# Kernel tuning notes

Hardware: AMD Instinct MI355X
Metric: run time of the kernel (lower is better)

The kernel has to match this reference:

```python
import jax, jax.numpy as jnp
import numpy as np

B, G, D, H = 8, 32, 768, 12
N = G * G
HD = D // H  # 64


def _make_rope(grid_size, head_dim):
    half = head_dim // 2
    inv_freq = 1.0 / (10000.0 ** (jnp.arange(0, half, 2, dtype=jnp.float32) / half))  # [half//2]
    pos = jnp.arange(grid_size, dtype=jnp.float32)[:, None] * inv_freq[None, :]       # [G, half//2]
    emb1 = jnp.concatenate([jnp.sin(pos), jnp.cos(pos)], axis=-1)                     # [G, half]
    emb_x = jnp.broadcast_to(emb1[None, :, :], (grid_size, grid_size, half))          # vary along x
    emb_y = jnp.broadcast_to(emb1[:, None, :], (grid_size, grid_size, half))          # vary along y
    emb = jnp.concatenate([emb_y, emb_x], axis=-1).reshape(grid_size * grid_size, head_dim)
    cos = jnp.cos(emb).reshape(1, grid_size * grid_size, 1, head_dim)
    sin = jnp.sin(emb).reshape(1, grid_size * grid_size, 1, head_dim)
    return cos, sin


def setup_inputs() -> dict:
    key = jax.random.key(0)
    kx, kw1, kb1, kw2, kb2 = jax.random.split(key, 5)
    x = jax.random.normal(kx, (B, N, D), dtype=jnp.float32)
    qkv_w = jax.random.normal(kw1, (3 * D, D), dtype=jnp.float32) * 0.02
    qkv_b = jax.random.normal(kb1, (3 * D,), dtype=jnp.float32) * 0.02
    proj_w = jax.random.normal(kw2, (D, D), dtype=jnp.float32) * 0.02
    proj_b = jax.random.normal(kb2, (D,), dtype=jnp.float32) * 0.02
    cos_emb, sin_emb = _make_rope(G, HD)
    return {"x": x, "qkv_w": qkv_w, "qkv_b": qkv_b, "proj_w": proj_w,
            "proj_b": proj_b, "cos_emb": cos_emb, "sin_emb": sin_emb}


def _apply_rope(t, cos, sin):
    # t: [B, N, H, HD]; cos/sin: [1, N, 1, HD]
    t1, t2 = t[..., 0::2], t[..., 1::2]
    rotated = jnp.concatenate([-t2, t1], axis=-1)
    return t * cos + rotated * sin


def reference(x, qkv_w, qkv_b, proj_w, proj_b, cos_emb, sin_emb):
    b, n, d = x.shape
    qkv = (x @ qkv_w.T + qkv_b).reshape(b, n, 3, H, HD)
    q, k, v = qkv[:, :, 0], qkv[:, :, 1], qkv[:, :, 2]  # [B, N, H, HD]
    q = _apply_rope(q, cos_emb, sin_emb)
    k = _apply_rope(k, cos_emb, sin_emb)
    scale = HD ** -0.5
    attn = jnp.einsum('bnhd,bmhd->bhnm', q, k) * scale
    attn = jax.nn.softmax(attn, axis=-1)
    out = jnp.einsum('bhnm,bmhd->bnhd', attn, v).reshape(b, n, d)
    return out @ proj_w.T + proj_b
```

## Files before the change

kernel.cpp:

```cpp
#include <hip/hip_runtime.h>
#include <stdint.h>
#include <stddef.h>

#define B_    8
#define NPOS  1024
#define DMODEL 768
#define NHEAD 12
#define HDIM  64
#define MTOK  (B_*NPOS)

typedef short bf16x8 __attribute__((ext_vector_type(8)));
typedef float f32x4  __attribute__((ext_vector_type(4)));

#if __has_builtin(__builtin_amdgcn_exp2f)
#define EXP2(x) __builtin_amdgcn_exp2f(x)
#else
#define EXP2(x) exp2f(x)
#endif

__device__ __forceinline__ unsigned short f2bs(float f) {
    unsigned int u = __builtin_bit_cast(unsigned int, f);
    u += 0x7FFFu + ((u >> 16) & 1u);
    return (unsigned short)(u >> 16);
}
__device__ __forceinline__ unsigned short f2bs_fast(float f) {
    unsigned int u = __builtin_bit_cast(unsigned int, f);
    return (unsigned short)((u + 0x8000u) >> 16);
}
__device__ __forceinline__ float bs2f(unsigned short s) {
    unsigned int u = ((unsigned int)s) << 16;
    return __builtin_bit_cast(float, u);
}

template<int N> __device__ __forceinline__ void vwait() {
    asm volatile("s_waitcnt vmcnt(%0)" :: "n"(N) : "memory");
}

__device__ __forceinline__ void gload16(const void* g, void* l) {
    __builtin_amdgcn_global_load_lds(
        (const __attribute__((address_space(1))) unsigned int*)g,
        (__attribute__((address_space(3))) unsigned int*)l, 16, 0, 0);
}

__global__ void cvt_all(const float* __restrict__ x, const float* __restrict__ w1,
                        const float* __restrict__ w2,
                        unsigned short* __restrict__ xb, unsigned short* __restrict__ wb,
                        unsigned short* __restrict__ pwb)
{
    const int N0 = MTOK * DMODEL / 4;
    const int N1 = 3 * DMODEL * DMODEL / 4;
    const int N2 = DMODEL * DMODEL / 4;
    int i = blockIdx.x * blockDim.x + threadIdx.x;
    int stride = gridDim.x * blockDim.x;
    for (; i < N0 + N1 + N2; i += stride) {
        const float4* s; unsigned short* d; int k;
        if (i < N0)            { s = (const float4*)x;  d = xb;  k = i; }
        else if (i < N0 + N1)  { s = (const float4*)w1; d = wb;  k = i - N0; }
        else                   { s = (const float4*)w2; d = pwb; k = i - N0 - N1; }
        float4 v = s[k];
        ushort4 o; o.x = f2bs(v.x); o.y = f2bs(v.y); o.z = f2bs(v.z); o.w = f2bs(v.w);
        ((ushort4*)d)[k] = o;
    }
}

__global__ __launch_bounds__(256)
void qkv_gemm_rope(const unsigned short* __restrict__ xb, const unsigned short* __restrict__ wb,
                   const float* __restrict__ bias, const float* __restrict__ cosE,
                   const float* __restrict__ sinE,
                   unsigned short* __restrict__ qb, unsigned short* __restrict__ kbuf,
                   unsigned short* __restrict__ vt)
{
    __shared__ char smem[65536];
    char* As0 = smem;
    char* Bs0 = smem + 16384;
    char* As1 = smem + 32768;
    char* Bs1 = smem + 49152;
    float* ct = (float*)smem;

    const int tid = threadIdx.x;
    const int lane = tid & 63, w = tid >> 6;
    const int wr = w >> 1, wc = w & 1;

    const int bid = blockIdx.x;
    const int xcd = bid & 7, idx = bid >> 3;
    const int n0 = (idx % 18) * 128;
    const int m0 = (xcd * 8 + idx / 18) * 128;

    const char* aS[4]; const char* bS[4]; int sDo[4];
    #pragma unroll
    for (int j = 0; j < 4; j++) {
        int i   = w * 4 + j;
        int row = i * 8 + (lane >> 3);
        int kb  = ((lane & 7) << 4) ^ ((row & 7) << 4);
        aS[j] = (const char*)(xb + (size_t)(m0 + row) * DMODEL) + kb;
        bS[j] = (const char*)(wb + (size_t)(n0 + row) * DMODEL) + kb;
        sDo[j] = i * 1024;
    }
    int aOf[2][4], bOf[2][4];
    #pragma unroll
    for (int kc = 0; kc < 2; kc++) {
        int chunk = kc * 4 + (lane >> 4);
        #pragma unroll
        for (int f = 0; f < 4; f++) {
            int ra = wr*64 + f*16 + (lane & 15);
            aOf[kc][f] = ra*128 + ((chunk << 4) ^ ((ra & 7) << 4));
            int rb = wc*64 + f*16 + (lane & 15);
            bOf[kc][f] = rb*128 + ((chunk << 4) ^ ((rb & 7) << 4));
        }
    }

    f32x4 acc[4][4];
    #pragma unroll
    for (int i = 0; i < 4; i++)
        #pragma unroll
        for (int j = 0; j < 4; j++) acc[i][j] = (f32x4){0.f, 0.f, 0.f, 0.f};

    auto gcompute = [&](char* Ac, char* Bc) {
        #pragma unroll
        for (int kc = 0; kc < 2; kc++) {
            bf16x8 af[4], bfr[4];
            #pragma unroll
            for (int mf = 0; mf < 4; mf++) af[mf] = *(const bf16x8*)(Ac + aOf[kc][mf]);
            #pragma unroll
            for (int nf = 0; nf < 4; nf++) bfr[nf] = *(const bf16x8*)(Bc + bOf[kc][nf]);
            #pragma unroll
            for (int mf = 0; mf < 4; mf++)
                #pragma unroll
                for (int nf = 0; nf < 4; nf++)
                    acc[mf][nf] = __builtin_amdgcn_mfma_f32_16x16x32_bf16(af[mf], bfr[nf], acc[mf][nf], 0, 0, 0);
        }
    };

#define QSTAGE(KOFF, AB, BB) do { \
    _Pragma("unroll") for (int j = 0; j < 4; j++) gload16(aS[j] + (KOFF), (AB) + sDo[j]); \
    _Pragma("unroll") for (int j = 0; j < 4; j++) gload16(bS[j] + (KOFF), (BB) + sDo[j]); \
} while (0)

    QSTAGE(0,   As0, Bs0);
    QSTAGE(128, As1, Bs1);

#define QSTEP(T, AC, BC, VM) \
    vwait<VM>(); \
    __builtin_amdgcn_s_barrier(); \
    gcompute(AC, BC); \
    __builtin_amdgcn_s_barrier(); \
    if ((T) + 2 < 12) QSTAGE(((T) + 2) * 128, AC, BC);

#define QPAIR(T, VM1) QSTEP(T, As0, Bs0, 8) QSTEP((T)+1, As1, Bs1, VM1)
    QPAIR(0, 8) QPAIR(2, 8) QPAIR(4, 8) QPAIR(6, 8) QPAIR(8, 8) QPAIR(10, 0)
#undef QPAIR
#undef QSTEP
#undef QSTAGE

    const int s  = n0 / DMODEL;
    const int h2 = (n0 % DMODEL) / 64;
    #pragma unroll
    for (int p = 0; p < 2; p++) {
        if (wr == p) {
            #pragma unroll
            for (int mf = 0; mf < 4; mf++)
                #pragma unroll
                for (int nf = 0; nf < 4; nf++) {
                    int c = wc*64 + nf*16 + (lane & 15);
                    float bv = bias[n0 + c];
                    #pragma unroll
                    for (int reg = 0; reg < 4; reg++) {
                        int r = mf*16 + ((lane >> 4) << 2) + reg;
                        ct[r*130 + c] = acc[mf][nf][reg] + bv;
                    }
                }
        }
        __syncthreads();
        const int rowg = m0 + p*64;
        const int bb   = rowg >> 10;
        const int pos0 = rowg & 1023;
        if (s < 2) {
            unsigned short* dst = (s == 0) ? qb : kbuf;
            const float qs = (s == 0) ? 0.125f * 1.44269504f : 1.0f;
            const int d = tid & 63, r0 = tid >> 6;
            for (int r = r0; r < 64; r += 4) {
                int pos = pos0 + r;
                float cv = cosE[pos*64 + d] * qs, sv = sinE[pos*64 + d] * qs;
                #pragma unroll
                for (int hh = 0; hh < 2; hh++) {
                    const float* rowp = ct + r*130 + hh*64;
                    float val = rowp[d];
                    float rot = (d < 32) ? -rowp[2*d + 1] : rowp[2*d - 64];
                    dst[(((size_t)(bb*NHEAD + h2 + hh))*NPOS + pos)*64 + d] = f2bs(val*cv + rot*sv);
                }
            }
        } else {
            const int posi = tid & 63, c0 = tid >> 6;
            for (int cc = c0; cc < 128; cc += 4) {
                int hh = cc >> 6, d = cc & 63;
                vt[(((size_t)(bb*NHEAD + h2 + hh))*64 + d)*NPOS + pos0 + posi] =
                    f2bs(ct[posi*130 + cc]);
            }
        }
        __syncthreads();
    }
}

__global__ __launch_bounds__(256)
void attn_mfma(const unsigned short* __restrict__ qb, const unsigned short* __restrict__ kbuf,
               const unsigned short* __restrict__ vt,
               unsigned short* __restrict__ att)
{
    __shared__ char smem[49152];
    char* Kb0 = smem;
    char* Kb1 = smem + 8192;
    char* Vb0 = smem + 16384;
    char* Vb1 = smem + 24576;
    char* Pq  = smem + 32768;

    const int tid = threadIdx.x;
    const int lane = tid & 63, w = tid >> 6;
    char* Pw = Pq + w * 4096;

    const int bid = blockIdx.x;
    const int swz = (bid & 7) * 96 + (bid >> 3);
    const int bh = swz >> 3, qt = swz & 7;
    const int bb = bh / NHEAD, hh = bh % NHEAD;
    const int q0 = qt * 128;

    const unsigned short* qp = qb   + (size_t)bh * NPOS * 64;
    const unsigned short* kp = kbuf + (size_t)bh * NPOS * 64;
    const unsigned short* vp = vt   + (size_t)bh * 64 * NPOS;

    const char* kS[2]; const char* vS[2]; int kvDo[2];
    #pragma unroll
    for (int j = 0; j < 2; j++) {
        int i   = w * 2 + j;
        int row = i * 8 + (lane >> 3);
        int kb  = ((lane & 7) << 4) ^ ((row & 7) << 4);
        kS[j] = (const char*)(kp) + (size_t)row * 128 + kb;
        vS[j] = (const char*)(vp) + (size_t)row * 2048 + kb;
        kvDo[j] = i * 1024;
    }
    int kOf[2][4], vOf[2][4], pOf[2][2];
    #pragma unroll
    for (int kc = 0; kc < 2; kc++) {
        int chunk = kc * 4 + (lane >> 4);
        #pragma unroll
        for (int f = 0; f < 4; f++) {
            int r = f*16 + (lane & 15);
            kOf[kc][f] = r*128 + ((chunk << 4) ^ ((r & 7) << 4));
            vOf[kc][f] = kOf[kc][f];
        }
        #pragma unroll
        for (int f = 0; f < 2; f++) {
            int r = f*16 + (lane & 15);
            pOf[kc][f] = r*128 + ((chunk << 4) ^ ((r & 7) << 4));
        }
    }

#define ASTAGE(T, KN, VN) do { \
    _Pragma("unroll") for (int j = 0; j < 2; j++) gload16(kS[j] + (size_t)(T) * 8192, (KN) + kvDo[j]); \
    _Pragma("unroll") for (int j = 0; j < 2; j++) gload16(vS[j] + (T) * 128,          (VN) + kvDo[j]); \
} while (0)

    #pragma unroll
    for (int j = 0; j < 4; j++) {
        int i   = w * 4 + j;
        int row = i * 8 + (lane >> 3);
        int kb  = ((lane & 7) << 4) ^ ((row & 7) << 4);
        gload16((const char*)(qp + (size_t)(q0 + row) * 64) + kb, Pq + i * 1024);
    }
    ASTAGE(0, Kb0, Vb0);
    vwait<4>();
    __builtin_amdgcn_s_barrier();
    bf16x8 qf[2][2];
    #pragma unroll
    for (int mf = 0; mf < 2; mf++)
        #pragma unroll
        for (int kc = 0; kc < 2; kc++)
            qf[mf][kc] = *(const bf16x8*)(Pq + w*4096 + pOf[kc][mf]);

    f32x4 O[2][4];
    float lpart[2][4];
    #pragma unroll
    for (int mf = 0; mf < 2; mf++)
        #pragma unroll
        for (int nd = 0; nd < 4; nd++) O[mf][nd] = (f32x4){0.f, 0.f, 0.f, 0.f};
    #pragma unroll
    for (int mf = 0; mf < 2; mf++)
        #pragma unroll
        for (int reg = 0; reg < 4; reg++) lpart[mf][reg] = 0.f;

    auto abody = [&](char* Kc, char* Vc) {
        f32x4 S[2][4];
        #pragma unroll
        for (int mf = 0; mf < 2; mf++)
            #pragma unroll
            for (int nf = 0; nf < 4; nf++) S[mf][nf] = (f32x4){0.f, 0.f, 0.f, 0.f};
        #pragma unroll
        for (int kc = 0; kc < 2; kc++) {
            bf16x8 kf[4];
            #pragma unroll
            for (int nf = 0; nf < 4; nf++) kf[nf] = *(const bf16x8*)(Kc + kOf[kc][nf]);
            __builtin_amdgcn_s_setprio(1);
            #pragma unroll
            for (int mf = 0; mf < 2; mf++)
                #pragma unroll
                for (int nf = 0; nf < 4; nf++)
                    S[mf][nf] = __builtin_amdgcn_mfma_f32_16x16x32_bf16(qf[mf][kc], kf[nf], S[mf][nf], 0, 0, 0);
            __builtin_amdgcn_s_setprio(0);
        }
        #pragma unroll
        for (int mf = 0; mf < 2; mf++) {
            #pragma unroll
            for (int reg = 0; reg < 4; reg++) {
                int ql = mf*16 + ((lane >> 4) << 2) + reg;
                #pragma unroll
                for (int nf = 0; nf < 4; nf++) {
                    float pv = EXP2(S[mf][nf][reg]);
                    lpart[mf][reg] += pv;
                    int key = nf*16 + (lane & 15);
                    *(unsigned short*)(Pw + ql*128 + ((key*2) ^ ((ql & 7) << 4))) = f2bs_fast(pv);
                }
            }
        }
        #pragma unroll
        for (int kc = 0; kc < 2; kc++) {
            bf16x8 pf[2], vf[4];
            #pragma unroll
            for (int mf = 0; mf < 2; mf++) pf[mf] = *(const bf16x8*)(Pw + pOf[kc][mf]);
            #pragma unroll
            for (int nd = 0; nd < 4; nd++) vf[nd] = *(const bf16x8*)(Vc + vOf[kc][nd]);
            __builtin_amdgcn_s_setprio(1);
            #pragma unroll
            for (int mf = 0; mf < 2; mf++)
                #pragma unroll
                for (int nd = 0; nd < 4; nd++)
                    O[mf][nd] = __builtin_amdgcn_mfma_f32_16x16x32_bf16(pf[mf], vf[nd], O[mf][nd], 0, 0, 0);
            __builtin_amdgcn_s_setprio(0);
        }
    };

#define ASTEP(T, KC, VC, KN, VN, VM) \
    if ((T) + 1 < 16) ASTAGE((T) + 1, KN, VN); \
    vwait<VM>(); \
    __builtin_amdgcn_s_barrier(); \
    abody(KC, VC); \
    __builtin_amdgcn_s_barrier();

#define APAIR(T, VM1) ASTEP(T, Kb0, Vb0, Kb1, Vb1, 4) ASTEP((T)+1, Kb1, Vb1, Kb0, Vb0, VM1)
    APAIR(0, 4) APAIR(2, 4) APAIR(4, 4) APAIR(6, 4)
    APAIR(8, 4) APAIR(10, 4) APAIR(12, 4) APAIR(14, 0)
#undef APAIR
#undef ASTEP
#undef ASTAGE

    #pragma unroll
    for (int mf = 0; mf < 2; mf++)
        #pragma unroll
        for (int reg = 0; reg < 4; reg++) {
            float l = lpart[mf][reg];
            l += __shfl_xor(l, 1);
            l += __shfl_xor(l, 2);
            l += __shfl_xor(l, 4);
            l += __shfl_xor(l, 8);
            float inv = 1.f / l;
            int qg = q0 + w*32 + mf*16 + ((lane >> 4) << 2) + reg;
            size_t rowb = ((size_t)bb * NPOS + qg) * DMODEL + hh * 64;
            #pragma unroll
            for (int nd = 0; nd < 4; nd++) {
                int d = nd*16 + (lane & 15);
                att[rowb + d] = f2bs(O[mf][nd][reg] * inv);
            }
        }
}

__global__ __launch_bounds__(256)
void proj_gemm(const unsigned short* __restrict__ a, const unsigned short* __restrict__ wgt,
               const float* __restrict__ bias, float* __restrict__ out)
{
    __shared__ char smem[65536];
    char* As0 = smem;
    char* Bs0 = smem + 16384;
    char* As1 = smem + 32768;
    char* Bs1 = smem + 49152;

    const int tid = threadIdx.x;
    const int lane = tid & 63, w = tid >> 6;
    const int wr = w >> 1, wc = w & 1;

    const int bid = blockIdx.x;
    const int xcd = bid & 7, idx = bid >> 3;
    const int n0 = (idx % 6) * 128;
    const int m0 = (xcd * 8 + idx / 6) * 128;

    const char* aS[4]; const char* bS[4]; int sDo[4];
    #pragma unroll
    for (int j = 0; j < 4; j++) {
        int i   = w * 4 + j;
        int row = i * 8 + (lane >> 3);
        int kb  = ((lane & 7) << 4) ^ ((row & 7) << 4);
        aS[j] = (const char*)(a   + (size_t)(m0 + row) * DMODEL) + kb;
        bS[j] = (const char*)(wgt + (size_t)(n0 + row) * DMODEL) + kb;
        sDo[j] = i * 1024;
    }
    int aOf[2][4], bOf[2][4];
    #pragma unroll
    for (int kc = 0; kc < 2; kc++) {
        int chunk = kc * 4 + (lane >> 4);
        #pragma unroll
        for (int f = 0; f < 4; f++) {
            int ra = wr*64 + f*16 + (lane & 15);
            aOf[kc][f] = ra*128 + ((chunk << 4) ^ ((ra & 7) << 4));
            int rb = wc*64 + f*16 + (lane & 15);
            bOf[kc][f] = rb*128 + ((chunk << 4) ^ ((rb & 7) << 4));
        }
    }

    f32x4 acc[4][4];
    #pragma unroll
    for (int i = 0; i < 4; i++)
        #pragma unroll
        for (int j = 0; j < 4; j++) acc[i][j] = (f32x4){0.f, 0.f, 0.f, 0.f};

    auto gcompute = [&](char* Ac, char* Bc) {
        #pragma unroll
        for (int kc = 0; kc < 2; kc++) {
            bf16x8 af[4], bfr[4];
            #pragma unroll
            for (int mf = 0; mf < 4; mf++) af[mf] = *(const bf16x8*)(Ac + aOf[kc][mf]);
            #pragma unroll
            for (int nf = 0; nf < 4; nf++) bfr[nf] = *(const bf16x8*)(Bc + bOf[kc][nf]);
            #pragma unroll
            for (int mf = 0; mf < 4; mf++)
                #pragma unroll
                for (int nf = 0; nf < 4; nf++)
                    acc[mf][nf] = __builtin_amdgcn_mfma_f32_16x16x32_bf16(af[mf], bfr[nf], acc[mf][nf], 0, 0, 0);
        }
    };

#define PSTAGE(KOFF, AB, BB) do { \
    _Pragma("unroll") for (int j = 0; j < 4; j++) gload16(aS[j] + (KOFF), (AB) + sDo[j]); \
    _Pragma("unroll") for (int j = 0; j < 4; j++) gload16(bS[j] + (KOFF), (BB) + sDo[j]); \
} while (0)

    PSTAGE(0,   As0, Bs0);
    PSTAGE(128, As1, Bs1);

#define PSTEP(T, AC, BC, VM) \
    vwait<VM>(); \
    __builtin_amdgcn_s_barrier(); \
    gcompute(AC, BC); \
    __builtin_amdgcn_s_barrier(); \
    if ((T) + 2 < 12) PSTAGE(((T) + 2) * 128, AC, BC);

#define PPAIR(T, VM1) PSTEP(T, As0, Bs0, 8) PSTEP((T)+1, As1, Bs1, VM1)
    PPAIR(0, 8) PPAIR(2, 8) PPAIR(4, 8) PPAIR(6, 8) PPAIR(8, 8) PPAIR(10, 0)
#undef PPAIR
#undef PSTEP
#undef PSTAGE

    #pragma unroll
    for (int mf = 0; mf < 4; mf++)
        #pragma unroll
        for (int nf = 0; nf < 4; nf++) {
            int c = n0 + wc*64 + nf*16 + (lane & 15);
            float bv = bias[c];
            #pragma unroll
            for (int reg = 0; reg < 4; reg++) {
                int r = m0 + wr*64 + mf*16 + ((lane >> 4) << 2) + reg;
                out[(size_t)r * DMODEL + c] = acc[mf][nf][reg] + bv;
            }
        }
}

extern "C" void kernel_launch(void* const* d_in, const int* in_sizes, int n_in,
                              void* d_out, int out_size, void* d_ws, size_t ws_size,
                              hipStream_t stream)
{
    (void)in_sizes; (void)n_in; (void)out_size; (void)ws_size;
    const float* x      = (const float*)d_in[0];
    const float* qkv_w  = (const float*)d_in[1];
    const float* qkv_b  = (const float*)d_in[2];
    const float* proj_w = (const float*)d_in[3];
    const float* proj_b = (const float*)d_in[4];
    const float* cosE   = (const float*)d_in[5];
    const float* sinE   = (const float*)d_in[6];
    float* out = (float*)d_out;

    char* ws = (char*)d_ws;
    unsigned short* xb  = (unsigned short*)(ws);
    unsigned short* wb  = (unsigned short*)(ws + 12582912);
    unsigned short* pwb = (unsigned short*)(ws + 16121856);
    unsigned short* qb  = (unsigned short*)(ws + 17301504);
    unsigned short* kbf = (unsigned short*)(ws + 29884416);
    unsigned short* vtp = (unsigned short*)(ws + 42467328);
    unsigned short* att = (unsigned short*)(ws + 55050240);

    cvt_all<<<2048, 256, 0, stream>>>(x, qkv_w, proj_w, xb, wb, pwb);
    qkv_gemm_rope<<<1152, 256, 0, stream>>>(xb, wb, qkv_b, cosE, sinE, qb, kbf, vtp);
    attn_mfma<<<768, 256, 0, stream>>>(qb, kbf, vtp, att);
    proj_gemm<<<384, 256, 0, stream>>>(att, pwb, proj_b, out);
}
```

Before: 120.9 us.

## Double block size to 512 threads with 256-row tiles across GEMMs and attention

```diff
diff --git a/kernel.cpp b/kernel.cpp
--- a/kernel.cpp
+++ b/kernel.cpp
@@ -63,18 +63,18 @@
     }
 }
 
-__global__ __launch_bounds__(256)
+__global__ __launch_bounds__(512, 2)
 void qkv_gemm_rope(const unsigned short* __restrict__ xb, const unsigned short* __restrict__ wb,
                    const float* __restrict__ bias, const float* __restrict__ cosE,
                    const float* __restrict__ sinE,
                    unsigned short* __restrict__ qb, unsigned short* __restrict__ kbuf,
                    unsigned short* __restrict__ vt)
 {
-    __shared__ char smem[65536];
+    __shared__ char smem[98304];
     char* As0 = smem;
-    char* Bs0 = smem + 16384;
-    char* As1 = smem + 32768;
-    char* Bs1 = smem + 49152;
+    char* Bs0 = smem + 32768;
+    char* As1 = smem + 49152;
+    char* Bs1 = smem + 81920;
     float* ct = (float*)smem;
 
     const int tid = threadIdx.x;
@@ -84,17 +84,25 @@
     const int bid = blockIdx.x;
     const int xcd = bid & 7, idx = bid >> 3;
     const int n0 = (idx % 18) * 128;
-    const int m0 = (xcd * 8 + idx / 18) * 128;
-
-    const char* aS[4]; const char* bS[4]; int sDo[4];
+    const int m0 = (xcd * 4 + idx / 18) * 256;
+
+    const char* aS[4]; int aDo[4];
     #pragma unroll
     for (int j = 0; j < 4; j++) {
         int i   = w * 4 + j;
         int row = i * 8 + (lane >> 3);
         int kb  = ((lane & 7) << 4) ^ ((row & 7) << 4);
         aS[j] = (const char*)(xb + (size_t)(m0 + row) * DMODEL) + kb;
+        aDo[j] = i * 1024;
+    }
+    const char* bS[2]; int bDo[2];
+    #pragma unroll
+    for (int j = 0; j < 2; j++) {
+        int i   = w * 2 + j;
+        int row = i * 8 + (lane >> 3);
+        int kb  = ((lane & 7) << 4) ^ ((row & 7) << 4);
         bS[j] = (const char*)(wb + (size_t)(n0 + row) * DMODEL) + kb;
-        sDo[j] = i * 1024;
+        bDo[j] = i * 1024;
     }
     int aOf[2][4], bOf[2][4];
     #pragma unroll
@@ -132,8 +140,8 @@
     };
 
 #define QSTAGE(KOFF, AB, BB) do { \
-    _Pragma("unroll") for (int j = 0; j < 4; j++) gload16(aS[j] + (KOFF), (AB) + sDo[j]); \
-    _Pragma("unroll") for (int j = 0; j < 4; j++) gload16(bS[j] + (KOFF), (BB) + sDo[j]); \
+    _Pragma("unroll") for (int j = 0; j < 4; j++) gload16(aS[j] + (KOFF), (AB) + aDo[j]); \
+    _Pragma("unroll") for (int j = 0; j < 2; j++) gload16(bS[j] + (KOFF), (BB) + bDo[j]); \
 } while (0)
 
     QSTAGE(0,   As0, Bs0);
@@ -146,8 +154,8 @@
     __builtin_amdgcn_s_barrier(); \
     if ((T) + 2 < 12) QSTAGE(((T) + 2) * 128, AC, BC);
 
-#define QPAIR(T, VM1) QSTEP(T, As0, Bs0, 8) QSTEP((T)+1, As1, Bs1, VM1)
-    QPAIR(0, 8) QPAIR(2, 8) QPAIR(4, 8) QPAIR(6, 8) QPAIR(8, 8) QPAIR(10, 0)
+#define QPAIR(T, VM1) QSTEP(T, As0, Bs0, 6) QSTEP((T)+1, As1, Bs1, VM1)
+    QPAIR(0, 6) QPAIR(2, 6) QPAIR(4, 6) QPAIR(6, 6) QPAIR(8, 6) QPAIR(10, 0)
 #undef QPAIR
 #undef QSTEP
 #undef QSTAGE
@@ -155,7 +163,7 @@
     const int s  = n0 / DMODEL;
     const int h2 = (n0 % DMODEL) / 64;
     #pragma unroll
-    for (int p = 0; p < 2; p++) {
+    for (int p = 0; p < 4; p++) {
         if (wr == p) {
             #pragma unroll
             for (int mf = 0; mf < 4; mf++)
@@ -178,7 +186,7 @@
             unsigned short* dst = (s == 0) ? qb : kbuf;
             const float qs = (s == 0) ? 0.125f * 1.44269504f : 1.0f;
             const int d = tid & 63, r0 = tid >> 6;
-            for (int r = r0; r < 64; r += 4) {
+            for (int r = r0; r < 64; r += 8) {
                 int pos = pos0 + r;
                 float cv = cosE[pos*64 + d] * qs, sv = sinE[pos*64 + d] * qs;
                 #pragma unroll
@@ -191,7 +199,7 @@
             }
         } else {
             const int posi = tid & 63, c0 = tid >> 6;
-            for (int cc = c0; cc < 128; cc += 4) {
+            for (int cc = c0; cc < 128; cc += 8) {
                 int hh = cc >> 6, d = cc & 63;
                 vt[(((size_t)(bb*NHEAD + h2 + hh))*64 + d)*NPOS + pos0 + posi] =
                     f2bs(ct[posi*130 + cc]);
@@ -201,12 +209,12 @@
     }
 }
 
-__global__ __launch_bounds__(256)
+__global__ __launch_bounds__(512, 4)
 void attn_mfma(const unsigned short* __restrict__ qb, const unsigned short* __restrict__ kbuf,
                const unsigned short* __restrict__ vt,
                unsigned short* __restrict__ att)
 {
-    __shared__ char smem[49152];
+    __shared__ char smem[65536];
     char* Kb0 = smem;
     char* Kb1 = smem + 8192;
     char* Vb0 = smem + 16384;
@@ -218,26 +226,24 @@
     char* Pw = Pq + w * 4096;
 
     const int bid = blockIdx.x;
-    const int swz = (bid & 7) * 96 + (bid >> 3);
-    const int bh = swz >> 3, qt = swz & 7;
+    const int swz = (bid & 7) * 48 + (bid >> 3);
+    const int bh = swz >> 2, qt = swz & 3;
     const int bb = bh / NHEAD, hh = bh % NHEAD;
-    const int q0 = qt * 128;
+    const int q0 = qt * 256;
 
     const unsigned short* qp = qb   + (size_t)bh * NPOS * 64;
     const unsigned short* kp = kbuf + (size_t)bh * NPOS * 64;
     const unsigned short* vp = vt   + (size_t)bh * 64 * NPOS;
 
-    const char* kS[2]; const char* vS[2]; int kvDo[2];
-    #pragma unroll
-    for (int j = 0; j < 2; j++) {
-        int i   = w * 2 + j;
-        int row = i * 8 + (lane >> 3);
+    const char* kS; const char* vS; int kvDo;
+    {
+        int row = w * 8 + (lane >> 3);
         int kb  = ((lane & 7) << 4) ^ ((row & 7) << 4);
-        kS[j] = (const char*)(kp) + (size_t)row * 128 + kb;
-        vS[j] = (const char*)(vp) + (size_t)row * 2048 + kb;
-        kvDo[j] = i * 1024;
-    }
-    int kOf[2][4], vOf[2][4], pOf[2][2];
+        kS = (const char*)(kp) + (size_t)row * 128 + kb;
+        vS = (const char*)(vp) + (size_t)row * 2048 + kb;
+        kvDo = w * 1024;
+    }
+    int kOf[2][4], pOf[2][2];
     #pragma unroll
     for (int kc = 0; kc < 2; kc++) {
         int chunk = kc * 4 + (lane >> 4);
@@ -245,7 +251,6 @@
         for (int f = 0; f < 4; f++) {
             int r = f*16 + (lane & 15);
             kOf[kc][f] = r*128 + ((chunk << 4) ^ ((r & 7) << 4));
-            vOf[kc][f] = kOf[kc][f];
         }
         #pragma unroll
         for (int f = 0; f < 2; f++) {
@@ -255,8 +260,8 @@
     }
 
 #define ASTAGE(T, KN, VN) do { \
-    _Pragma("unroll") for (int j = 0; j < 2; j++) gload16(kS[j] + (size_t)(T) * 8192, (KN) + kvDo[j]); \
-    _Pragma("unroll") for (int j = 0; j < 2; j++) gload16(vS[j] + (T) * 128,          (VN) + kvDo[j]); \
+    gload16(kS + (size_t)(T) * 8192, (KN) + kvDo); \
+    gload16(vS + (T) * 128,          (VN) + kvDo); \
 } while (0)
 
     #pragma unroll
@@ -267,7 +272,7 @@
         gload16((const char*)(qp + (size_t)(q0 + row) * 64) + kb, Pq + i * 1024);
     }
     ASTAGE(0, Kb0, Vb0);
-    vwait<4>();
+    vwait<2>();
     __builtin_amdgcn_s_barrier();
     bf16x8 qf[2][2];
     #pragma unroll
@@ -326,7 +331,7 @@
             #pragma unroll
             for (int mf = 0; mf < 2; mf++) pf[mf] = *(const bf16x8*)(Pw + pOf[kc][mf]);
             #pragma unroll
-            for (int nd = 0; nd < 4; nd++) vf[nd] = *(const bf16x8*)(Vc + vOf[kc][nd]);
+            for (int nd = 0; nd < 4; nd++) vf[nd] = *(const bf16x8*)(Vc + kOf[kc][nd]);
             __builtin_amdgcn_s_setprio(1);
             #pragma unroll
             for (int mf = 0; mf < 2; mf++)
@@ -344,9 +349,9 @@
     abody(KC, VC); \
     __builtin_amdgcn_s_barrier();
 
-#define APAIR(T, VM1) ASTEP(T, Kb0, Vb0, Kb1, Vb1, 4) ASTEP((T)+1, Kb1, Vb1, Kb0, Vb0, VM1)
-    APAIR(0, 4) APAIR(2, 4) APAIR(4, 4) APAIR(6, 4)
-    APAIR(8, 4) APAIR(10, 4) APAIR(12, 4) APAIR(14, 0)
+#define APAIR(T, VM1) ASTEP(T, Kb0, Vb0, Kb1, Vb1, 2) ASTEP((T)+1, Kb1, Vb1, Kb0, Vb0, VM1)
+    APAIR(0, 2) APAIR(2, 2) APAIR(4, 2) APAIR(6, 2)
+    APAIR(8, 2) APAIR(10, 2) APAIR(12, 2) APAIR(14, 0)
 #undef APAIR
 #undef ASTEP
 #undef ASTAGE
@@ -371,15 +376,15 @@
         }
 }
 
-__global__ __launch_bounds__(256)
+__global__ __launch_bounds__(512, 2)
 void proj_gemm(const unsigned short* __restrict__ a, const unsigned short* __restrict__ wgt,
                const float* __restrict__ bias, float* __restrict__ out)
 {
-    __shared__ char smem[65536];
+    __shared__ char smem[98304];
     char* As0 = smem;
-    char* Bs0 = smem + 16384;
-    char* As1 = smem + 32768;
-    char* Bs1 = smem + 49152;
+    char* Bs0 = smem + 32768;
+    char* As1 = smem + 49152;
+    char* Bs1 = smem + 81920;
 
     const int tid = threadIdx.x;
     const int lane = tid & 63, w = tid >> 6;
@@ -388,17 +393,25 @@
     const int bid = blockIdx.x;
     const int xcd = bid & 7, idx = bid >> 3;
     const int n0 = (idx % 6) * 128;
-    const int m0 = (xcd * 8 + idx / 6) * 128;
-
-    const char* aS[4]; const char* bS[4]; int sDo[4];
+    const int m0 = (xcd * 4 + idx / 6) * 256;
+
+    const char* aS[4]; int aDo[4];
     #pragma unroll
     for (int j = 0; j < 4; j++) {
         int i   = w * 4 + j;
         int row = i * 8 + (lane >> 3);
         int kb  = ((lane & 7) << 4) ^ ((row & 7) << 4);
-        aS[j] = (const char*)(a   + (size_t)(m0 + row) * DMODEL) + kb;
+        aS[j] = (const char*)(a + (size_t)(m0 + row) * DMODEL) + kb;
+        aDo[j] = i * 1024;
+    }
+    const char* bS[2]; int bDo[2];
+    #pragma unroll
+    for (int j = 0; j < 2; j++) {
+        int i   = w * 2 + j;
+        int row = i * 8 + (lane >> 3);
+        int kb  = ((lane & 7) << 4) ^ ((row & 7) << 4);
         bS[j] = (const char*)(wgt + (size_t)(n0 + row) * DMODEL) + kb;
-        sDo[j] = i * 1024;
+        bDo[j] = i * 1024;
     }
     int aOf[2][4], bOf[2][4];
     #pragma unroll
@@ -436,8 +449,8 @@
     };
 
 #define PSTAGE(KOFF, AB, BB) do { \
-    _Pragma("unroll") for (int j = 0; j < 4; j++) gload16(aS[j] + (KOFF), (AB) + sDo[j]); \
-    _Pragma("unroll") for (int j = 0; j < 4; j++) gload16(bS[j] + (KOFF), (BB) + sDo[j]); \
+    _Pragma("unroll") for (int j = 0; j < 4; j++) gload16(aS[j] + (KOFF), (AB) + aDo[j]); \
+    _Pragma("unroll") for (int j = 0; j < 2; j++) gload16(bS[j] + (KOFF), (BB) + bDo[j]); \
 } while (0)
 
     PSTAGE(0,   As0, Bs0);
@@ -450,8 +463,8 @@
     __builtin_amdgcn_s_barrier(); \
     if ((T) + 2 < 12) PSTAGE(((T) + 2) * 128, AC, BC);
 
-#define PPAIR(T, VM1) PSTEP(T, As0, Bs0, 8) PSTEP((T)+1, As1, Bs1, VM1)
-    PPAIR(0, 8) PPAIR(2, 8) PPAIR(4, 8) PPAIR(6, 8) PPAIR(8, 8) PPAIR(10, 0)
+#define PPAIR(T, VM1) PSTEP(T, As0, Bs0, 6) PSTEP((T)+1, As1, Bs1, VM1)
+    PPAIR(0, 6) PPAIR(2, 6) PPAIR(4, 6) PPAIR(6, 6) PPAIR(8, 6) PPAIR(10, 0)
 #undef PPAIR
 #undef PSTEP
 #undef PSTAGE
@@ -494,7 +507,7 @@
     unsigned short* att = (unsigned short*)(ws + 55050240);
 
     cvt_all<<<2048, 256, 0, stream>>>(x, qkv_w, proj_w, xb, wb, pwb);
-    qkv_gemm_rope<<<1152, 256, 0, stream>>>(xb, wb, qkv_b, cosE, sinE, qb, kbf, vtp);
-    attn_mfma<<<768, 256, 0, stream>>>(qb, kbf, vtp, att);
-    proj_gemm<<<384, 256, 0, stream>>>(att, pwb, proj_b, out);
-}
+    qkv_gemm_rope<<<576, 512, 0, stream>>>(xb, wb, qkv_b, cosE, sinE, qb, kbf, vtp);
+    attn_mfma<<<384, 512, 0, stream>>>(qb, kbf, vtp, att);
+    proj_gemm<<<192, 512, 0, stream>>>(att, pwb, proj_b, out);
+}
```

New measurement: 191.2 us. 1.58x slower.

## Fuse fp32-to-bf16 conversion of x into QKV GEMM A-tile loading

Applied to the files above, without the earlier changes.

```diff
diff --git a/kernel.cpp b/kernel.cpp
--- a/kernel.cpp
+++ b/kernel.cpp
@@ -32,6 +32,16 @@
     return __builtin_bit_cast(float, u);
 }
 
+__device__ __forceinline__ unsigned int pack2(float a, float b) {
+    unsigned int ua = __builtin_bit_cast(unsigned int, a) + 0x8000u;
+    unsigned int ub = __builtin_bit_cast(unsigned int, b) + 0x8000u;
+#if __has_builtin(__builtin_amdgcn_perm)
+    return __builtin_amdgcn_perm(ub, ua, 0x07060302);
+#else
+    return (ua >> 16) | (ub & 0xFFFF0000u);
+#endif
+}
+
 template<int N> __device__ __forceinline__ void vwait() {
     asm volatile("s_waitcnt vmcnt(%0)" :: "n"(N) : "memory");
 }
@@ -42,29 +52,25 @@
         (__attribute__((address_space(3))) unsigned int*)l, 16, 0, 0);
 }
 
-__global__ void cvt_all(const float* __restrict__ x, const float* __restrict__ w1,
-                        const float* __restrict__ w2,
-                        unsigned short* __restrict__ xb, unsigned short* __restrict__ wb,
-                        unsigned short* __restrict__ pwb)
+__global__ void cvt_w(const float* __restrict__ w1, const float* __restrict__ w2,
+                      unsigned short* __restrict__ wb, unsigned short* __restrict__ pwb)
 {
-    const int N0 = MTOK * DMODEL / 4;
     const int N1 = 3 * DMODEL * DMODEL / 4;
     const int N2 = DMODEL * DMODEL / 4;
     int i = blockIdx.x * blockDim.x + threadIdx.x;
     int stride = gridDim.x * blockDim.x;
-    for (; i < N0 + N1 + N2; i += stride) {
+    for (; i < N1 + N2; i += stride) {
         const float4* s; unsigned short* d; int k;
-        if (i < N0)            { s = (const float4*)x;  d = xb;  k = i; }
-        else if (i < N0 + N1)  { s = (const float4*)w1; d = wb;  k = i - N0; }
-        else                   { s = (const float4*)w2; d = pwb; k = i - N0 - N1; }
+        if (i < N1) { s = (const float4*)w1; d = wb;  k = i; }
+        else        { s = (const float4*)w2; d = pwb; k = i - N1; }
         float4 v = s[k];
         ushort4 o; o.x = f2bs(v.x); o.y = f2bs(v.y); o.z = f2bs(v.z); o.w = f2bs(v.w);
         ((ushort4*)d)[k] = o;
     }
 }
 
-__global__ __launch_bounds__(256)
-void qkv_gemm_rope(const unsigned short* __restrict__ xb, const unsigned short* __restrict__ wb,
+__global__ __launch_bounds__(256, 2)
+void qkv_gemm_rope(const float* __restrict__ x, const unsigned short* __restrict__ wb,
                    const float* __restrict__ bias, const float* __restrict__ cosE,
                    const float* __restrict__ sinE,
                    unsigned short* __restrict__ qb, unsigned short* __restrict__ kbuf,
@@ -86,15 +92,22 @@
     const int n0 = (idx % 18) * 128;
     const int m0 = (xcd * 8 + idx / 18) * 128;
 
-    const char* aS[4]; const char* bS[4]; int sDo[4];
+    const float* aS[4]; int aLds[4];
+    #pragma unroll
+    for (int j = 0; j < 4; j++) {
+        int i   = w * 4 + j;
+        int row = i * 8 + (lane >> 3);
+        aS[j]   = x + (size_t)(m0 + row) * DMODEL + (lane & 7) * 8;
+        aLds[j] = row * 128 + (((lane & 7) * 16) ^ ((row & 7) << 4));
+    }
+    const char* bS[4]; int bDo[4];
     #pragma unroll
     for (int j = 0; j < 4; j++) {
         int i   = w * 4 + j;
         int row = i * 8 + (lane >> 3);
         int kb  = ((lane & 7) << 4) ^ ((row & 7) << 4);
-        aS[j] = (const char*)(xb + (size_t)(m0 + row) * DMODEL) + kb;
         bS[j] = (const char*)(wb + (size_t)(n0 + row) * DMODEL) + kb;
-        sDo[j] = i * 1024;
+        bDo[j] = i * 1024;
     }
     int aOf[2][4], bOf[2][4];
     #pragma unroll
@@ -115,6 +128,8 @@
         #pragma unroll
         for (int j = 0; j < 4; j++) acc[i][j] = (f32x4){0.f, 0.f, 0.f, 0.f};
 
+    float4 ar[4][2];
+
     auto gcompute = [&](char* Ac, char* Bc) {
         #pragma unroll
         for (int kc = 0; kc < 2; kc++) {
@@ -131,26 +146,48 @@
         }
     };
 
-#define QSTAGE(KOFF, AB, BB) do { \
-    _Pragma("unroll") for (int j = 0; j < 4; j++) gload16(aS[j] + (KOFF), (AB) + sDo[j]); \
-    _Pragma("unroll") for (int j = 0; j < 4; j++) gload16(bS[j] + (KOFF), (BB) + sDo[j]); \
+#define ALOAD(T) do { \
+    _Pragma("unroll") for (int j = 0; j < 4; j++) { \
+        ar[j][0] = *(const float4*)(aS[j] + (T) * 64); \
+        ar[j][1] = *(const float4*)(aS[j] + (T) * 64 + 4); } \
 } while (0)
 
-    QSTAGE(0,   As0, Bs0);
-    QSTAGE(128, As1, Bs1);
-
-#define QSTEP(T, AC, BC, VM) \
-    vwait<VM>(); \
-    __builtin_amdgcn_s_barrier(); \
+#define AWRITE(AB) do { \
+    _Pragma("unroll") for (int j = 0; j < 4; j++) { \
+        uint4 pv; \
+        pv.x = pack2(ar[j][0].x, ar[j][0].y); \
+        pv.y = pack2(ar[j][0].z, ar[j][0].w); \
+        pv.z = pack2(ar[j][1].x, ar[j][1].y); \
+        pv.w = pack2(ar[j][1].z, ar[j][1].w); \
+        *(uint4*)((AB) + aLds[j]) = pv; } \
+} while (0)
+
+#define BSTAGE(T, BB) do { \
+    _Pragma("unroll") for (int j = 0; j < 4; j++) gload16(bS[j] + (T) * 128, (BB) + bDo[j]); \
+} while (0)
+
+    ALOAD(0); BSTAGE(0, Bs0);
+    vwait<4>();
+    AWRITE(As0);
+    ALOAD(1); BSTAGE(1, Bs1);
+    __syncthreads();
+
+#define QSTEP(T, AC, BC, AN) \
     gcompute(AC, BC); \
     __builtin_amdgcn_s_barrier(); \
-    if ((T) + 2 < 12) QSTAGE(((T) + 2) * 128, AC, BC);
-
-#define QPAIR(T, VM1) QSTEP(T, As0, Bs0, 8) QSTEP((T)+1, As1, Bs1, VM1)
-    QPAIR(0, 8) QPAIR(2, 8) QPAIR(4, 8) QPAIR(6, 8) QPAIR(8, 8) QPAIR(10, 0)
+    vwait<0>(); \
+    if ((T) + 1 < 12) AWRITE(AN); \
+    if ((T) + 2 < 12) { ALOAD((T) + 2); BSTAGE((T) + 2, BC); } \
+    asm volatile("s_waitcnt lgkmcnt(0)" ::: "memory"); \
+    __builtin_amdgcn_s_barrier();
+
+#define QPAIR(T) QSTEP(T, As0, Bs0, As1) QSTEP((T)+1, As1, Bs1, As0)
+    QPAIR(0) QPAIR(2) QPAIR(4) QPAIR(6) QPAIR(8) QPAIR(10)
 #undef QPAIR
 #undef QSTEP
-#undef QSTAGE
+#undef BSTAGE
+#undef AWRITE
+#undef ALOAD
 
     const int s  = n0 / DMODEL;
     const int h2 = (n0 % DMODEL) / 64;
@@ -237,7 +274,7 @@
         vS[j] = (const char*)(vp) + (size_t)row * 2048 + kb;
         kvDo[j] = i * 1024;
     }
-    int kOf[2][4], vOf[2][4], pOf[2][2];
+    int kOf[2][4], pOf[2][2];
     #pragma unroll
     for (int kc = 0; kc < 2; kc++) {
         int chunk = kc * 4 + (lane >> 4);
@@ -245,7 +282,6 @@
         for (int f = 0; f < 4; f++) {
             int r = f*16 + (lane & 15);
             kOf[kc][f] = r*128 + ((chunk << 4) ^ ((r & 7) << 4));
-            vOf[kc][f] = kOf[kc][f];
         }
         #pragma unroll
         for (int f = 0; f < 2; f++) {
@@ -326,7 +362,7 @@
             #pragma unroll
             for (int mf = 0; mf < 2; mf++) pf[mf] = *(const bf16x8*)(Pw + pOf[kc][mf]);
             #pragma unroll
-            for (int nd = 0; nd < 4; nd++) vf[nd] = *(const bf16x8*)(Vc + vOf[kc][nd]);
+            for (int nd = 0; nd < 4; nd++) vf[nd] = *(const bf16x8*)(Vc + kOf[kc][nd]);
             __builtin_amdgcn_s_setprio(1);
             #pragma unroll
             for (int mf = 0; mf < 2; mf++)
@@ -485,16 +521,15 @@
     float* out = (float*)d_out;
 
     char* ws = (char*)d_ws;
-    unsigned short* xb  = (unsigned short*)(ws);
-    unsigned short* wb  = (unsigned short*)(ws + 12582912);
-    unsigned short* pwb = (unsigned short*)(ws + 16121856);
-    unsigned short* qb  = (unsigned short*)(ws + 17301504);
-    unsigned short* kbf = (unsigned short*)(ws + 29884416);
-    unsigned short* vtp = (unsigned short*)(ws + 42467328);
-    unsigned short* att = (unsigned short*)(ws + 55050240);
-
-    cvt_all<<<2048, 256, 0, stream>>>(x, qkv_w, proj_w, xb, wb, pwb);
-    qkv_gemm_rope<<<1152, 256, 0, stream>>>(xb, wb, qkv_b, cosE, sinE, qb, kbf, vtp);
+    unsigned short* wb  = (unsigned short*)(ws);
+    unsigned short* pwb = (unsigned short*)(ws + 3538944);
+    unsigned short* qb  = (unsigned short*)(ws + 4718592);
+    unsigned short* kbf = (unsigned short*)(ws + 17301504);
+    unsigned short* vtp = (unsigned short*)(ws + 29884416);
+    unsigned short* att = (unsigned short*)(ws + 42467328);
+
+    cvt_w<<<1024, 256, 0, stream>>>(qkv_w, proj_w, wb, pwb);
+    qkv_gemm_rope<<<1152, 256, 0, stream>>>(x, wb, qkv_b, cosE, sinE, qb, kbf, vtp);
     attn_mfma<<<768, 256, 0, stream>>>(qb, kbf, vtp, att);
     proj_gemm<<<384, 256, 0, stream>>>(att, pwb, proj_b, out);
 }
```

Result: slower. 134.6 us (+11.3%).

## Enlarge QKV GEMM tile to 256x128 with 512 threads and triple-buffered LDS

Applied to the files above, without the earlier changes.

```diff
diff --git a/kernel.cpp b/kernel.cpp
--- a/kernel.cpp
+++ b/kernel.cpp
@@ -63,18 +63,17 @@
     }
 }
 
-__global__ __launch_bounds__(256)
+__global__ __launch_bounds__(512, 2)
 void qkv_gemm_rope(const unsigned short* __restrict__ xb, const unsigned short* __restrict__ wb,
                    const float* __restrict__ bias, const float* __restrict__ cosE,
                    const float* __restrict__ sinE,
                    unsigned short* __restrict__ qb, unsigned short* __restrict__ kbuf,
                    unsigned short* __restrict__ vt)
 {
-    __shared__ char smem[65536];
-    char* As0 = smem;
-    char* Bs0 = smem + 16384;
-    char* As1 = smem + 32768;
-    char* Bs1 = smem + 49152;
+    __shared__ char smem[147456];
+    char* b0 = smem;
+    char* b1 = smem + 49152;
+    char* b2 = smem + 98304;
     float* ct = (float*)smem;
 
     const int tid = threadIdx.x;
@@ -84,17 +83,25 @@
     const int bid = blockIdx.x;
     const int xcd = bid & 7, idx = bid >> 3;
     const int n0 = (idx % 18) * 128;
-    const int m0 = (xcd * 8 + idx / 18) * 128;
-
-    const char* aS[4]; const char* bS[4]; int sDo[4];
+    const int m0 = (xcd * 4 + idx / 18) * 256;
+
+    const char* aS[4]; int aDo[4];
     #pragma unroll
     for (int j = 0; j < 4; j++) {
         int i   = w * 4 + j;
         int row = i * 8 + (lane >> 3);
         int kb  = ((lane & 7) << 4) ^ ((row & 7) << 4);
         aS[j] = (const char*)(xb + (size_t)(m0 + row) * DMODEL) + kb;
+        aDo[j] = i * 1024;
+    }
+    const char* bS[2]; int bDo[2];
+    #pragma unroll
+    for (int j = 0; j < 2; j++) {
+        int i   = w * 2 + j;
+        int row = i * 8 + (lane >> 3);
+        int kb  = ((lane & 7) << 4) ^ ((row & 7) << 4);
         bS[j] = (const char*)(wb + (size_t)(n0 + row) * DMODEL) + kb;
-        sDo[j] = i * 1024;
+        bDo[j] = i * 1024;
     }
     int aOf[2][4], bOf[2][4];
     #pragma unroll
@@ -115,47 +122,80 @@
         #pragma unroll
         for (int j = 0; j < 4; j++) acc[i][j] = (f32x4){0.f, 0.f, 0.f, 0.f};
 
-    auto gcompute = [&](char* Ac, char* Bc) {
-        #pragma unroll
-        for (int kc = 0; kc < 2; kc++) {
-            bf16x8 af[4], bfr[4];
-            #pragma unroll
-            for (int mf = 0; mf < 4; mf++) af[mf] = *(const bf16x8*)(Ac + aOf[kc][mf]);
-            #pragma unroll
-            for (int nf = 0; nf < 4; nf++) bfr[nf] = *(const bf16x8*)(Bc + bOf[kc][nf]);
-            #pragma unroll
-            for (int mf = 0; mf < 4; mf++)
-                #pragma unroll
-                for (int nf = 0; nf < 4; nf++)
-                    acc[mf][nf] = __builtin_amdgcn_mfma_f32_16x16x32_bf16(af[mf], bfr[nf], acc[mf][nf], 0, 0, 0);
-        }
+    auto phaseK = [&](int kc, char* cur, char* nb, bool dostage, int koff) {
+        bf16x8 af[4], bfr[4];
+        #pragma unroll
+        for (int f = 0; f < 4; f++) {
+            af[f]  = *(const bf16x8*)(cur + aOf[kc][f]);
+            bfr[f] = *(const bf16x8*)(cur + 32768 + bOf[kc][f]);
+        }
+        if (dostage) {
+            if (kc == 0) {
+                gload16(aS[0] + koff, nb + aDo[0]);
+                gload16(aS[1] + koff, nb + aDo[1]);
+                gload16(bS[0] + koff, nb + 32768 + bDo[0]);
+            } else {
+                gload16(aS[2] + koff, nb + aDo[2]);
+                gload16(aS[3] + koff, nb + aDo[3]);
+                gload16(bS[1] + koff, nb + 32768 + bDo[1]);
+            }
+        }
+        __builtin_amdgcn_s_barrier();
+        __builtin_amdgcn_s_setprio(1);
+        #pragma unroll
+        for (int mf = 0; mf < 4; mf++)
+            #pragma unroll
+            for (int nf = 0; nf < 4; nf++)
+                acc[mf][nf] = __builtin_amdgcn_mfma_f32_16x16x32_bf16(af[mf], bfr[nf], acc[mf][nf], 0, 0, 0);
+        __builtin_amdgcn_s_setprio(0);
     };
 
-#define QSTAGE(KOFF, AB, BB) do { \
-    _Pragma("unroll") for (int j = 0; j < 4; j++) gload16(aS[j] + (KOFF), (AB) + sDo[j]); \
-    _Pragma("unroll") for (int j = 0; j < 4; j++) gload16(bS[j] + (KOFF), (BB) + sDo[j]); \
-} while (0)
-
-    QSTAGE(0,   As0, Bs0);
-    QSTAGE(128, As1, Bs1);
-
-#define QSTEP(T, AC, BC, VM) \
-    vwait<VM>(); \
+    auto stage6 = [&](int koff, char* buf) {
+        gload16(aS[0] + koff, buf + aDo[0]);
+        gload16(aS[1] + koff, buf + aDo[1]);
+        gload16(bS[0] + koff, buf + 32768 + bDo[0]);
+        gload16(aS[2] + koff, buf + aDo[2]);
+        gload16(aS[3] + koff, buf + aDo[3]);
+        gload16(bS[1] + koff, buf + 32768 + bDo[1]);
+    };
+
+    stage6(0,   b0);
+    stage6(128, b1);
+    vwait<6>();
+    __builtin_amdgcn_s_barrier();
+
+#define QTSTEP(T, CUR, NB, VMN) \
+    phaseK(0, CUR, NB, (T) + 2 < 12, ((T) + 2) * 128); \
     __builtin_amdgcn_s_barrier(); \
-    gcompute(AC, BC); \
+    phaseK(1, CUR, NB, (T) + 2 < 12, ((T) + 2) * 128); \
+    vwait<VMN>(); \
+    __builtin_amdgcn_s_barrier();
+
+#define QTSTEP_LAST(T, CUR) \
+    phaseK(0, CUR, CUR, false, 0); \
     __builtin_amdgcn_s_barrier(); \
-    if ((T) + 2 < 12) QSTAGE(((T) + 2) * 128, AC, BC);
-
-#define QPAIR(T, VM1) QSTEP(T, As0, Bs0, 8) QSTEP((T)+1, As1, Bs1, VM1)
-    QPAIR(0, 8) QPAIR(2, 8) QPAIR(4, 8) QPAIR(6, 8) QPAIR(8, 8) QPAIR(10, 0)
-#undef QPAIR
-#undef QSTEP
-#undef QSTAGE
+    phaseK(1, CUR, CUR, false, 0); \
+    __builtin_amdgcn_s_barrier();
+
+    QTSTEP(0,  b0, b2, 6)
+    QTSTEP(1,  b1, b0, 6)
+    QTSTEP(2,  b2, b1, 6)
+    QTSTEP(3,  b0, b2, 6)
+    QTSTEP(4,  b1, b0, 6)
+    QTSTEP(5,  b2, b1, 6)
+    QTSTEP(6,  b0, b2, 6)
+    QTSTEP(7,  b1, b0, 6)
+    QTSTEP(8,  b2, b1, 6)
+    QTSTEP(9,  b0, b2, 6)
+    QTSTEP(10, b1, b2, 0)
+    QTSTEP_LAST(11, b2)
+#undef QTSTEP
+#undef QTSTEP_LAST
 
     const int s  = n0 / DMODEL;
     const int h2 = (n0 % DMODEL) / 64;
     #pragma unroll
-    for (int p = 0; p < 2; p++) {
+    for (int p = 0; p < 4; p++) {
         if (wr == p) {
             #pragma unroll
             for (int mf = 0; mf < 4; mf++)
@@ -178,7 +218,7 @@
             unsigned short* dst = (s == 0) ? qb : kbuf;
             const float qs = (s == 0) ? 0.125f * 1.44269504f : 1.0f;
             const int d = tid & 63, r0 = tid >> 6;
-            for (int r = r0; r < 64; r += 4) {
+            for (int r = r0; r < 64; r += 8) {
                 int pos = pos0 + r;
                 float cv = cosE[pos*64 + d] * qs, sv = sinE[pos*64 + d] * qs;
                 #pragma unroll
@@ -191,7 +231,7 @@
             }
         } else {
             const int posi = tid & 63, c0 = tid >> 6;
-            for (int cc = c0; cc < 128; cc += 4) {
+            for (int cc = c0; cc < 128; cc += 8) {
                 int hh = cc >> 6, d = cc & 63;
                 vt[(((size_t)(bb*NHEAD + h2 + hh))*64 + d)*NPOS + pos0 + posi] =
                     f2bs(ct[posi*130 + cc]);
@@ -237,7 +277,7 @@
         vS[j] = (const char*)(vp) + (size_t)row * 2048 + kb;
         kvDo[j] = i * 1024;
     }
-    int kOf[2][4], vOf[2][4], pOf[2][2];
+    int kOf[2][4], pOf[2][2];
     #pragma unroll
     for (int kc = 0; kc < 2; kc++) {
         int chunk = kc * 4 + (lane >> 4);
@@ -245,7 +285,6 @@
         for (int f = 0; f < 4; f++) {
             int r = f*16 + (lane & 15);
             kOf[kc][f] = r*128 + ((chunk << 4) ^ ((r & 7) << 4));
-            vOf[kc][f] = kOf[kc][f];
         }
         #pragma unroll
         for (int f = 0; f < 2; f++) {
@@ -326,7 +365,7 @@
             #pragma unroll
             for (int mf = 0; mf < 2; mf++) pf[mf] = *(const bf16x8*)(Pw + pOf[kc][mf]);
             #pragma unroll
-            for (int nd = 0; nd < 4; nd++) vf[nd] = *(const bf16x8*)(Vc + vOf[kc][nd]);
+            for (int nd = 0; nd < 4; nd++) vf[nd] = *(const bf16x8*)(Vc + kOf[kc][nd]);
             __builtin_amdgcn_s_setprio(1);
             #pragma unroll
             for (int mf = 0; mf < 2; mf++)
@@ -494,7 +533,7 @@
     unsigned short* att = (unsigned short*)(ws + 55050240);
 
     cvt_all<<<2048, 256, 0, stream>>>(x, qkv_w, proj_w, xb, wb, pwb);
-    qkv_gemm_rope<<<1152, 256, 0, stream>>>(xb, wb, qkv_b, cosE, sinE, qb, kbf, vtp);
+    qkv_gemm_rope<<<576, 512, 0, stream>>>(xb, wb, qkv_b, cosE, sinE, qb, kbf, vtp);
     attn_mfma<<<768, 256, 0, stream>>>(qb, kbf, vtp, att);
     proj_gemm<<<384, 256, 0, stream>>>(att, pwb, proj_b, out);
 }
```

Result: slower. 128.2 us (+6.1%).
